# Performance work log

Hardware: AMD Instinct MI355X
Metric: run time of the kernel (lower is better)

Reference implementation:

```python
import jax, jax.numpy as jnp
import numpy as np

NEG = -1e9  # stand-in for -inf in masked softmax (safe under autodiff)

def setup_inputs() -> dict:
    key = jax.random.key(0)
    ks = jax.random.split(key, 10)
    B, Btot, O, M, F, Dsrc, Ddst = 32, 64, 1000, 100, 32, 6, 3
    raw_opes = jax.random.normal(ks[0], (B, O, Dsrc), jnp.float32)
    raw_mas = jax.random.normal(ks[1], (B, M, Ddst), jnp.float32)
    proc_time = jax.random.uniform(ks[2], (B, O, M), jnp.float32)
    ope_ma_adj = jax.random.randint(ks[3], (Btot, O, M), 0, 2).astype(jnp.int64)
    batch_idxes = jnp.sort(jax.random.randint(ks[4], (B,), 0, Btot)).astype(jnp.int64)
    # xavier-ish scaled params
    W_src = jax.random.normal(ks[5], (Dsrc, F), jnp.float32) * (2.0 / np.sqrt(Dsrc + F))
    W_dst = jax.random.normal(ks[6], (Ddst, F), jnp.float32) * (2.0 / np.sqrt(Ddst + F))
    W_edge = jax.random.normal(ks[7], (F,), jnp.float32) * (2.0 / np.sqrt(1 + F))
    attn_l = jax.random.normal(ks[8], (F,), jnp.float32) * (2.0 / np.sqrt(1 + F))
    attn_r = jax.random.normal(ks[9], (F,), jnp.float32) * (2.0 / np.sqrt(1 + F))
    return {"raw_opes": raw_opes, "raw_mas": raw_mas, "proc_time": proc_time,
            "ope_ma_adj": ope_ma_adj, "batch_idxes": batch_idxes,
            "W_src": W_src, "W_dst": W_dst, "W_edge": W_edge,
            "attn_l": attn_l, "attn_r": attn_r}

def _leaky(x, s=0.2):
    return jnp.where(x >= 0, x, s * x)

def reference(raw_opes, raw_mas, proc_time, ope_ma_adj, batch_idxes, W_src, W_dst, W_edge, attn_l, attn_r):
    adj = ope_ma_adj[batch_idxes]                      # [B,O,M] int
    adjf = adj.astype(raw_opes.dtype)
    feat_src = raw_opes @ W_src                        # [B,O,F]
    feat_dst = raw_mas @ W_dst                         # [B,M,F]
    feat_edge = proc_time[..., None] * W_edge          # [B,O,M,F]
    el = feat_src @ attn_l                             # [B,O]
    er = feat_dst @ attn_r                             # [B,M]
    ee = feat_edge @ attn_l                            # [B,O,M]  (original uses attn_l for edges)
    a = adjf * el[:, :, None] + ee + adjf * er[:, None, :]   # [B,O,M]
    eijk = _leaky(a)                                   # [B,O,M]
    ekk = _leaky(er + er)                              # [B,M]
    e = jnp.concatenate([eijk, ekk[:, None, :]], axis=1)     # [B,O+1,M]
    mask = jnp.concatenate([adj == 1, jnp.ones_like(adj[:, :1, :], dtype=bool)], axis=1)
    e = jnp.where(mask, e, NEG)
    alpha = jax.nn.softmax(e, axis=1)                  # softmax over ope dim (+self)
    alpha_ijk = alpha[:, :-1, :]                       # [B,O,M]
    alpha_kk = alpha[:, -1, :]                         # [B,M]
    Wmu_ijk = feat_edge + feat_src[:, :, None, :]      # [B,O,M,F]
    b = jnp.einsum('bomf,bom->bmf', Wmu_ijk, alpha_ijk)
    c = feat_dst * alpha_kk[..., None]
    return jax.nn.sigmoid(b + c)                       # [B,M,F]
```

## Files before the change

kernel.cpp:

```cpp
#include <hip/hip_runtime.h>

#define B_DIM 32
#define O_DIM 1000
#define M_DIM 100
#define F_DIM 32
#define DS 6
#define DD 3
#define SEG 25
#define CHUNK 40
#define OSUB 10
#define TRIPS 4
#define MT 25

__global__ __launch_bounds__(256) void gat_partial(
    const float* __restrict__ raw_opes,
    const float* __restrict__ raw_mas,
    const float* __restrict__ proc_time,
    const int*   __restrict__ adj,
    const int*   __restrict__ bidx,
    const float* __restrict__ Wsrc,
    const float* __restrict__ Wdst,
    const float* __restrict__ Wedge,
    const float* __restrict__ attn_l,
    const float* __restrict__ attn_r,
    float* __restrict__ partial)
{
    const int b   = blockIdx.x / SEG;
    const int seg = blockIdx.x % SEG;
    const int t   = threadIdx.x;
    const int o0  = seg * CHUNK;

    __shared__ float ro_s[CHUNK * DS];
    __shared__ float part_s[OSUB][M_DIM][9];

    const float* rop = raw_opes + ((size_t)b * O_DIM + o0) * DS;
    if (t < CHUNK * DS) ro_s[t] = rop[t];

    float wl[DS] = {0, 0, 0, 0, 0, 0};
    float we = 0.f;
    for (int f = 0; f < F_DIM; ++f) {
        float al = attn_l[f];
        we = fmaf(Wedge[f], al, we);
        #pragma unroll
        for (int d = 0; d < DS; ++d) wl[d] = fmaf(Wsrc[d * F_DIM + f], al, wl[d]);
    }
    float wr[DD] = {0, 0, 0};
    for (int f = 0; f < F_DIM; ++f) {
        float ar = attn_r[f];
        #pragma unroll
        for (int d = 0; d < DD; ++d) wr[d] = fmaf(Wdst[d * F_DIM + f], ar, wr[d]);
    }
    __syncthreads();

    if (t < 25 * OSUB) {
        const int mg = t % 25;
        const int g  = t / 25;

        const float* ptp = proc_time + ((size_t)b * O_DIM + o0) * M_DIM + mg * 4;
        const int*   adp = adj + ((size_t)bidx[b] * O_DIM + o0) * M_DIM + mg * 4;

        float4 pt[TRIPS];
        int4   av[TRIPS];
        #pragma unroll
        for (int k = 0; k < TRIPS; ++k) {
            const int row = g + k * OSUB;
            pt[k] = *(const float4*)(ptp + row * M_DIM);
            av[k] = *(const int4*)(adp + row * M_DIM);
        }

        const float* rm = raw_mas + ((size_t)b * M_DIM + mg * 4) * DD;
        float4 er;
        er.x = fmaf(rm[0], wr[0], fmaf(rm[1],  wr[1], rm[2]  * wr[2]));
        er.y = fmaf(rm[3], wr[0], fmaf(rm[4],  wr[1], rm[5]  * wr[2]));
        er.z = fmaf(rm[6], wr[0], fmaf(rm[7],  wr[1], rm[8]  * wr[2]));
        er.w = fmaf(rm[9], wr[0], fmaf(rm[10], wr[1], rm[11] * wr[2]));

        float4 den = make_float4(0, 0, 0, 0), spa = make_float4(0, 0, 0, 0);
        float4 sd[DS];
        #pragma unroll
        for (int d = 0; d < DS; ++d) sd[d] = make_float4(0, 0, 0, 0);

        #pragma unroll
        for (int k = 0; k < TRIPS; ++k) {
            const int row = g + k * OSUB;
            float ro[DS];
            #pragma unroll
            for (int d = 0; d < DS; ++d) ro[d] = ro_s[row * DS + d];
            float elr = 0.f;
            #pragma unroll
            for (int d = 0; d < DS; ++d) elr = fmaf(ro[d], wl[d], elr);

            float s0 = elr + er.x + we * pt[k].x;
            float s1 = elr + er.y + we * pt[k].y;
            float s2 = elr + er.z + we * pt[k].z;
            float s3 = elr + er.w + we * pt[k].w;
            s0 = fmaxf(s0, 0.2f * s0); s1 = fmaxf(s1, 0.2f * s1);
            s2 = fmaxf(s2, 0.2f * s2); s3 = fmaxf(s3, 0.2f * s3);
            float p0 = (av[k].x == 1) ? __expf(s0) : 0.f;
            float p1 = (av[k].y == 1) ? __expf(s1) : 0.f;
            float p2 = (av[k].z == 1) ? __expf(s2) : 0.f;
            float p3 = (av[k].w == 1) ? __expf(s3) : 0.f;
            den.x += p0; den.y += p1; den.z += p2; den.w += p3;
            spa.x = fmaf(p0, pt[k].x, spa.x); spa.y = fmaf(p1, pt[k].y, spa.y);
            spa.z = fmaf(p2, pt[k].z, spa.z); spa.w = fmaf(p3, pt[k].w, spa.w);
            #pragma unroll
            for (int d = 0; d < DS; ++d) {
                sd[d].x = fmaf(p0, ro[d], sd[d].x);
                sd[d].y = fmaf(p1, ro[d], sd[d].y);
                sd[d].z = fmaf(p2, ro[d], sd[d].z);
                sd[d].w = fmaf(p3, ro[d], sd[d].w);
            }
        }

        #pragma unroll
        for (int j = 0; j < 4; ++j) {
            const int m = mg * 4 + j;
            float* ps = part_s[g][m];
            ps[0] = j == 0 ? den.x : j == 1 ? den.y : j == 2 ? den.z : den.w;
            ps[1] = j == 0 ? spa.x : j == 1 ? spa.y : j == 2 ? spa.z : spa.w;
            #pragma unroll
            for (int d = 0; d < DS; ++d)
                ps[2 + d] = j == 0 ? sd[d].x : j == 1 ? sd[d].y : j == 2 ? sd[d].z : sd[d].w;
        }
    }
    __syncthreads();

    if (t < 2 * M_DIM) {
        const int m = t % M_DIM, half = t / M_DIM;
        float a[4] = {0, 0, 0, 0};
        #pragma unroll
        for (int g = 0; g < OSUB; ++g) {
            #pragma unroll
            for (int k = 0; k < 4; ++k) a[k] += part_s[g][m][half * 4 + k];
        }
        *(float4*)(partial + (((size_t)b * SEG + seg) * M_DIM + m) * 8 + half * 4) =
            make_float4(a[0], a[1], a[2], a[3]);
    }
}

__global__ __launch_bounds__(256) void gat_final(
    const float* __restrict__ raw_mas,
    const float* __restrict__ Wsrc,
    const float* __restrict__ Wdst,
    const float* __restrict__ Wedge,
    const float* __restrict__ attn_r,
    const float* __restrict__ partial,
    float* __restrict__ out)
{
    const int b  = blockIdx.x >> 2;
    const int m0 = (blockIdx.x & 3) * MT;
    const int t  = threadIdx.x;

    __shared__ float smd[MT][9];

    if (t < MT * 8) {
        const int ml = t % MT;
        const int k  = t / MT;
        const float* p = partial + (((size_t)b * SEG) * M_DIM + m0 + ml) * 8 + k;
        float acc = 0.f;
        #pragma unroll
        for (int s = 0; s < SEG; ++s) acc += p[(size_t)s * M_DIM * 8];
        smd[ml][k] = acc;
    }
    __syncthreads();

    if (t < MT) {
        float wr[DD] = {0, 0, 0};
        for (int f = 0; f < F_DIM; ++f) {
            float ar = attn_r[f];
            #pragma unroll
            for (int d = 0; d < DD; ++d) wr[d] = fmaf(Wdst[d * F_DIM + f], ar, wr[d]);
        }
        const float* rm = raw_mas + ((size_t)b * M_DIM + m0 + t) * DD;
        float er = fmaf(rm[0], wr[0], fmaf(rm[1], wr[1], rm[2] * wr[2]));
        float skk = 2.f * er;
        skk = fmaxf(skk, 0.2f * skk);
        float pkk = __expf(skk);
        float den = smd[t][0], spa = smd[t][1];
        float s0 = smd[t][2], s1 = smd[t][3], s2 = smd[t][4],
              s3 = smd[t][5], s4 = smd[t][6], s5 = smd[t][7];
        float inv = 1.f / (den + pkk);
        smd[t][0] = s0 * inv; smd[t][1] = s1 * inv; smd[t][2] = s2 * inv;
        smd[t][3] = s3 * inv; smd[t][4] = s4 * inv; smd[t][5] = s5 * inv;
        smd[t][6] = spa * inv;
        smd[t][7] = pkk * inv;
    }
    __syncthreads();

    for (int idx = t; idx < MT * F_DIM; idx += 256) {
        const int ml = idx >> 5;
        const int f  = idx & 31;
        float v = smd[ml][6] * Wedge[f];
        #pragma unroll
        for (int d = 0; d < DS; ++d) v = fmaf(smd[ml][d], Wsrc[d * F_DIM + f], v);
        const float* rm = raw_mas + ((size_t)b * M_DIM + m0 + ml) * DD;
        float fd = 0.f;
        #pragma unroll
        for (int d = 0; d < DD; ++d) fd = fmaf(rm[d], Wdst[d * F_DIM + f], fd);
        v = fmaf(fd, smd[ml][7], v);
        out[((size_t)b * M_DIM + m0 + ml) * F_DIM + f] = 1.f / (1.f + __expf(-v));
    }
}

extern "C" void kernel_launch(void* const* d_in, const int* in_sizes, int n_in,
                              void* d_out, int out_size, void* d_ws, size_t ws_size,
                              hipStream_t stream) {
    const float* raw_opes  = (const float*)d_in[0];
    const float* raw_mas   = (const float*)d_in[1];
    const float* proc_time = (const float*)d_in[2];
    const int*   adj       = (const int*)d_in[3];
    const int*   bidx      = (const int*)d_in[4];
    const float* Wsrc      = (const float*)d_in[5];
    const float* Wdst      = (const float*)d_in[6];
    const float* Wedge     = (const float*)d_in[7];
    const float* attn_l    = (const float*)d_in[8];
    const float* attn_r    = (const float*)d_in[9];
    float* out     = (float*)d_out;
    float* partial = (float*)d_ws;

    gat_partial<<<B_DIM * SEG, 256, 0, stream>>>(raw_opes, raw_mas, proc_time, adj, bidx,
                                                 Wsrc, Wdst, Wedge, attn_l, attn_r, partial);
    gat_final<<<B_DIM * 4, 256, 0, stream>>>(raw_mas, Wsrc, Wdst, Wedge, attn_r, partial, out);
}
```

Baseline: 19.10 us.

## Fuse final reduction into partial kernel via last-block atomic counter

```diff
diff --git a/kernel.cpp b/kernel.cpp
--- a/kernel.cpp
+++ b/kernel.cpp
@@ -10,9 +10,9 @@
 #define CHUNK 40
 #define OSUB 10
 #define TRIPS 4
-#define MT 25
-
-__global__ __launch_bounds__(256) void gat_partial(
+#define PART_FLOATS ((size_t)B_DIM * SEG * M_DIM * 8)
+
+__global__ __launch_bounds__(256) void gat_fused(
     const float* __restrict__ raw_opes,
     const float* __restrict__ raw_mas,
     const float* __restrict__ proc_time,
@@ -23,7 +23,9 @@
     const float* __restrict__ Wedge,
     const float* __restrict__ attn_l,
     const float* __restrict__ attn_r,
-    float* __restrict__ partial)
+    float* __restrict__ partial,
+    int*   __restrict__ cnt,
+    float* __restrict__ out)
 {
     const int b   = blockIdx.x / SEG;
     const int seg = blockIdx.x % SEG;
@@ -32,6 +34,23 @@
 
     __shared__ float ro_s[CHUNK * DS];
     __shared__ float part_s[OSUB][M_DIM][9];
+    __shared__ int   flag_s;
+
+    const int mg = t % 25;
+    const int g  = t / 25;
+
+    float4 pt[TRIPS];
+    int4   av[TRIPS];
+    if (t < 25 * OSUB) {
+        const float* ptp = proc_time + ((size_t)b * O_DIM + o0) * M_DIM + mg * 4;
+        #pragma unroll
+        for (int k = 0; k < TRIPS; ++k)
+            pt[k] = *(const float4*)(ptp + (g + k * OSUB) * M_DIM);
+        const int* adp = adj + ((size_t)bidx[b] * O_DIM + o0) * M_DIM + mg * 4;
+        #pragma unroll
+        for (int k = 0; k < TRIPS; ++k)
+            av[k] = *(const int4*)(adp + (g + k * OSUB) * M_DIM);
+    }
 
     const float* rop = raw_opes + ((size_t)b * O_DIM + o0) * DS;
     if (t < CHUNK * DS) ro_s[t] = rop[t];
@@ -53,21 +72,6 @@
     __syncthreads();
 
     if (t < 25 * OSUB) {
-        const int mg = t % 25;
-        const int g  = t / 25;
-
-        const float* ptp = proc_time + ((size_t)b * O_DIM + o0) * M_DIM + mg * 4;
-        const int*   adp = adj + ((size_t)bidx[b] * O_DIM + o0) * M_DIM + mg * 4;
-
-        float4 pt[TRIPS];
-        int4   av[TRIPS];
-        #pragma unroll
-        for (int k = 0; k < TRIPS; ++k) {
-            const int row = g + k * OSUB;
-            pt[k] = *(const float4*)(ptp + row * M_DIM);
-            av[k] = *(const int4*)(adp + row * M_DIM);
-        }
-
         const float* rm = raw_mas + ((size_t)b * M_DIM + mg * 4) * DD;
         float4 er;
         er.x = fmaf(rm[0], wr[0], fmaf(rm[1],  wr[1], rm[2]  * wr[2]));
@@ -129,49 +133,45 @@
         const int m = t % M_DIM, half = t / M_DIM;
         float a[4] = {0, 0, 0, 0};
         #pragma unroll
-        for (int g = 0; g < OSUB; ++g) {
-            #pragma unroll
-            for (int k = 0; k < 4; ++k) a[k] += part_s[g][m][half * 4 + k];
+        for (int gg = 0; gg < OSUB; ++gg) {
+            #pragma unroll
+            for (int k = 0; k < 4; ++k) a[k] += part_s[gg][m][half * 4 + k];
         }
         *(float4*)(partial + (((size_t)b * SEG + seg) * M_DIM + m) * 8 + half * 4) =
             make_float4(a[0], a[1], a[2], a[3]);
     }
-}
-
-__global__ __launch_bounds__(256) void gat_final(
-    const float* __restrict__ raw_mas,
-    const float* __restrict__ Wsrc,
-    const float* __restrict__ Wdst,
-    const float* __restrict__ Wedge,
-    const float* __restrict__ attn_r,
-    const float* __restrict__ partial,
-    float* __restrict__ out)
-{
-    const int b  = blockIdx.x >> 2;
-    const int m0 = (blockIdx.x & 3) * MT;
-    const int t  = threadIdx.x;
-
-    __shared__ float smd[MT][9];
-
-    if (t < MT * 8) {
-        const int ml = t % MT;
-        const int k  = t / MT;
-        const float* p = partial + (((size_t)b * SEG) * M_DIM + m0 + ml) * 8 + k;
-        float acc = 0.f;
-        #pragma unroll
-        for (int s = 0; s < SEG; ++s) acc += p[(size_t)s * M_DIM * 8];
-        smd[ml][k] = acc;
-    }
-    __syncthreads();
-
-    if (t < MT) {
-        float wr[DD] = {0, 0, 0};
-        for (int f = 0; f < F_DIM; ++f) {
-            float ar = attn_r[f];
-            #pragma unroll
-            for (int d = 0; d < DD; ++d) wr[d] = fmaf(Wdst[d * F_DIM + f], ar, wr[d]);
-        }
-        const float* rm = raw_mas + ((size_t)b * M_DIM + m0 + t) * DD;
+    __syncthreads();
+
+    if (t == 0) {
+        __threadfence();
+        int old = __hip_atomic_fetch_add(cnt + b, 1, __ATOMIC_ACQ_REL,
+                                         __HIP_MEMORY_SCOPE_AGENT);
+        flag_s = (old == SEG - 1);
+    }
+    __syncthreads();
+    if (!flag_s) return;
+
+    __threadfence();
+    float (*smd)[9] = part_s[0];
+
+    if (t < 2 * M_DIM) {
+        const int m = t % M_DIM, half = t / M_DIM;
+        const float* p = partial + ((size_t)b * SEG * M_DIM + m) * 8 + half * 4;
+        float4 acc = make_float4(0, 0, 0, 0);
+        #pragma unroll
+        for (int s = 0; s < SEG; ++s) {
+            float4 x = *(const float4*)(p + (size_t)s * M_DIM * 8);
+            acc.x += x.x; acc.y += x.y; acc.z += x.z; acc.w += x.w;
+        }
+        smd[m][half * 4 + 0] = acc.x;
+        smd[m][half * 4 + 1] = acc.y;
+        smd[m][half * 4 + 2] = acc.z;
+        smd[m][half * 4 + 3] = acc.w;
+    }
+    __syncthreads();
+
+    if (t < M_DIM) {
+        const float* rm = raw_mas + ((size_t)b * M_DIM + t) * DD;
         float er = fmaf(rm[0], wr[0], fmaf(rm[1], wr[1], rm[2] * wr[2]));
         float skk = 2.f * er;
         skk = fmaxf(skk, 0.2f * skk);
@@ -187,18 +187,18 @@
     }
     __syncthreads();
 
-    for (int idx = t; idx < MT * F_DIM; idx += 256) {
-        const int ml = idx >> 5;
-        const int f  = idx & 31;
-        float v = smd[ml][6] * Wedge[f];
-        #pragma unroll
-        for (int d = 0; d < DS; ++d) v = fmaf(smd[ml][d], Wsrc[d * F_DIM + f], v);
-        const float* rm = raw_mas + ((size_t)b * M_DIM + m0 + ml) * DD;
+    for (int idx = t; idx < M_DIM * F_DIM; idx += 256) {
+        const int m = idx >> 5;
+        const int f = idx & 31;
+        float v = smd[m][6] * Wedge[f];
+        #pragma unroll
+        for (int d = 0; d < DS; ++d) v = fmaf(smd[m][d], Wsrc[d * F_DIM + f], v);
+        const float* rm = raw_mas + ((size_t)b * M_DIM + m) * DD;
         float fd = 0.f;
         #pragma unroll
         for (int d = 0; d < DD; ++d) fd = fmaf(rm[d], Wdst[d * F_DIM + f], fd);
-        v = fmaf(fd, smd[ml][7], v);
-        out[((size_t)b * M_DIM + m0 + ml) * F_DIM + f] = 1.f / (1.f + __expf(-v));
+        v = fmaf(fd, smd[m][7], v);
+        out[((size_t)b * M_DIM + m) * F_DIM + f] = 1.f / (1.f + __expf(-v));
     }
 }
 
@@ -217,8 +217,10 @@
     const float* attn_r    = (const float*)d_in[9];
     float* out     = (float*)d_out;
     float* partial = (float*)d_ws;
-
-    gat_partial<<<B_DIM * SEG, 256, 0, stream>>>(raw_opes, raw_mas, proc_time, adj, bidx,
-                                                 Wsrc, Wdst, Wedge, attn_l, attn_r, partial);
-    gat_final<<<B_DIM * 4, 256, 0, stream>>>(raw_mas, Wsrc, Wdst, Wedge, attn_r, partial, out);
+    int*   cnt     = (int*)((char*)d_ws + PART_FLOATS * sizeof(float));
+
+    hipMemsetAsync(cnt, 0, B_DIM * sizeof(int), stream);
+    gat_fused<<<B_DIM * SEG, 256, 0, stream>>>(raw_opes, raw_mas, proc_time, adj, bidx,
+                                               Wsrc, Wdst, Wedge, attn_l, attn_r,
+                                               partial, cnt, out);
 }
```

Result: slower. 75.60 us (+295.8%).
